# Performance work log

Hardware: AMD Instinct MI355X
Metric: run time of the kernel (lower is better)

Reference implementation:

```python
import jax, jax.numpy as jnp
import numpy as np

H = 512        # edge_feature_size (input_size == hidden_size)
B = 8          # batch
N = 8192       # n_nodes


def setup_inputs() -> dict:
    key = jax.random.key(0)
    k1, k2, k3, k4 = jax.random.split(key, 4)
    # Glorot-ish init scale like torch GRU (uniform +-1/sqrt(H))
    s = 1.0 / np.sqrt(H)
    e_wv = jax.random.normal(k1, (B, H, N), dtype=jnp.float32)
    m_wv = jax.random.normal(k2, (B, H, N), dtype=jnp.float32)
    # torch GRU weight layout: [3H, H] stacked as (reset, update, new)
    W_ih = jax.random.uniform(k3, (3 * H, H), dtype=jnp.float32, minval=-s, maxval=s)
    W_hh = jax.random.uniform(k4, (3 * H, H), dtype=jnp.float32, minval=-s, maxval=s)
    return {"e_wv": e_wv, "m_wv": m_wv, "W_ih": W_ih, "W_hh": W_hh}


def reference(e_wv, m_wv, W_ih, W_hh):
    # Single-step GRU cell (no bias), applied to all nodes at once.
    # e_wv: hidden state h0 [B, H, N]; m_wv: input x [B, H, N].
    gi = jnp.einsum('gh,bhn->bgn', W_ih, m_wv)   # [B, 3H, N]
    gh = jnp.einsum('gh,bhn->bgn', W_hh, e_wv)   # [B, 3H, N]
    i_r, i_z, i_n = gi[:, :H], gi[:, H:2 * H], gi[:, 2 * H:]
    h_r, h_z, h_n = gh[:, :H], gh[:, H:2 * H], gh[:, 2 * H:]
    r = jax.nn.sigmoid(i_r + h_r)
    z = jax.nn.sigmoid(i_z + h_z)
    n = jnp.tanh(i_n + r * h_n)
    return (1.0 - z) * n + z * e_wv              # [B, H, N]
```

## Files before the change

kernel.cpp:

```cpp
#include <hip/hip_runtime.h>
#include <hip/hip_bf16.h>


#define HH 512
#define NBATCH 8
#define NN 8192
#define BN 128
#define BK 64
#define NSTEPS 16
#define THREADS 256
#define A_BYTES (192 * BK * 2)
#define B_BYTES (BN * 128)
#define BUF_BYTES (A_BYTES + B_BYTES)
#define LDS_TOTAL (2 * BUF_BYTES)

#define WIMG_BYTES (NBATCH * NSTEPS * 12288 * 2)
#define XIMG_BYTES ((size_t)NBATCH * NSTEPS * 64 * 16384)
#define WS_NEED (WIMG_BYTES + XIMG_BYTES)

typedef __attribute__((ext_vector_type(8))) short short8;
typedef __attribute__((ext_vector_type(4))) float f32x4;

__device__ __forceinline__ unsigned cvt_pk_bf16(float a, float b) {
  unsigned r;
  asm("v_cvt_pk_bf16_f32 %0, %1, %2" : "=v"(r) : "v"(a), "v"(b));
  return r;
}

__device__ __forceinline__ void gload_lds16(const void* g, void* l) {
  __builtin_amdgcn_global_load_lds(
      (__attribute__((address_space(1))) void*)(g),
      (__attribute__((address_space(3))) void*)(l), 16, 0, 0);
}

#define MFMA16(a_, b_, c_) __builtin_amdgcn_mfma_f32_16x16x32_bf16((a_), (b_), (c_), 0, 0, 0)

#define BARRIER_FENCED() do {                               \
    __builtin_amdgcn_sched_barrier(0);                      \
    __builtin_amdgcn_s_barrier();                           \
    __builtin_amdgcn_sched_barrier(0);                      \
  } while (0)

__global__ void prepack_w(const float* __restrict__ W_ih, const float* __restrict__ W_hh,
                          __hip_bfloat16* __restrict__ ws) {
  int t = blockIdx.x * 256 + threadIdx.x;
  int blk = t / 12288;
  int e = t % 12288;
  int ra = e >> 6;
  int kk = (e & 63) ^ ((ra & 7) << 3);
  int gate = ra >> 6;
  int h = (blk >> 4) * 64 + (ra & 63);
  int row = gate * HH + h;
  int kg = (blk & 15) * 64 + kk;
  float v = (kg < 512) ? W_ih[row * 512 + kg] : W_hh[row * 512 + (kg - 512)];
  ws[t] = __float2bfloat16(v);
}

__global__ void prepack_x(const float* __restrict__ e_wv, const float* __restrict__ m_wv,
                          char* __restrict__ ximg) {
  __shared__ __align__(16) char tile[16384];
  const int tid = threadIdx.x;
  const int idx = blockIdx.x;
  const int b  = idx >> 10;
  const int s  = (idx >> 6) & 15;
  const int nt = idx & 63;
  const float* src = (s < 8 ? m_wv : e_wv)
                   + (size_t)b * HH * NN + (size_t)(64 * (s & 7)) * NN + nt * 128;
#pragma unroll
  for (int it = 0; it < 8; ++it) {
    int g = it * 256 + tid;
    int k = g >> 5;
    int n4 = (g & 31) << 2;
    f32x4 v = *(const f32x4*)(src + (size_t)k * NN + n4);
#pragma unroll
    for (int j = 0; j < 4; ++j) {
      int n = n4 + j;
      int byteoff = n * 128 + ((2 * k) ^ (((n >> 1) & 7) << 4));
      *(__hip_bfloat16*)(tile + byteoff) = __float2bfloat16(v[j]);
    }
  }
  __syncthreads();
  char* dst = ximg + (size_t)idx * 16384;
#pragma unroll
  for (int it = 0; it < 4; ++it) {
    int p = it * 4096 + tid * 16;
    *(uint4*)(dst + p) = *(const uint4*)(tile + p);
  }
}

__global__ __launch_bounds__(THREADS, 2)
void gru_main_dma(const float* __restrict__ e_wv,
                  const __hip_bfloat16* __restrict__ wimg,
                  const char* __restrict__ ximg, float* __restrict__ out) {
  extern __shared__ char smem[];
  const int tid  = threadIdx.x;
  const int lane = tid & 63;
  const int wave = tid >> 6;
  const int wm = wave >> 1;
  const int wn = wave & 1;

  const int wg  = blockIdx.x;
  const int swz = (wg & 7) * 512 + (wg >> 3);
  const int ht  = swz & 7;
  const int nt  = (swz >> 3) & 63;
  const int b   = swz >> 9;

  const size_t batch_off = (size_t)b * HH * NN;
  const char* wA  = (const char*)wimg + (size_t)ht * NSTEPS * A_BYTES + tid * 16;
  const char* xib = ximg + ((size_t)(b * 16) * 64 + nt) * 16384 + tid * 16;

  f32x4 acc_r[2][4]  = {};
  f32x4 acc_z[2][4]  = {};
  f32x4 acc_in[2][4] = {};
  f32x4 acc_hn[2][4] = {};

  int aoff[2], boff[2];
#pragma unroll
  for (int kb2 = 0; kb2 < 2; ++kb2) {
    const int K = kb2 * 64 + ((lane >> 4) << 4);
    aoff[kb2] = (wm * 32 + (lane & 15)) * 128 + (K ^ ((lane & 7) << 4));
    boff[kb2] = A_BYTES + (wn * 64 + (lane & 15)) * 128
              + (K ^ (((lane >> 1) & 7) << 4));
  }

  auto stage = [&](int t, char* buf) {
    const char* gA = wA + (size_t)t * A_BYTES;
    char* lA = buf + tid * 16;
#pragma unroll
    for (int i = 0; i < 6; ++i)
      gload_lds16(gA + i * 4096, lA + i * 4096);
    const char* gB = xib + (size_t)t * (64 * 16384);
    char* lB = buf + A_BYTES + tid * 16;
#pragma unroll
    for (int i = 0; i < 4; ++i)
      gload_lds16(gB + i * 4096, lB + i * 4096);
  };
  auto compute_kb2 = [&](const char* cb, int kb2, bool firstHalf) {
    short8 bfr[4];
#pragma unroll
    for (int ni = 0; ni < 4; ++ni)
      bfr[ni] = *(const short8*)(cb + boff[kb2] + ni * 2048);
    {
      short8 a0 = *(const short8*)(cb + aoff[kb2]);
      short8 a1 = *(const short8*)(cb + aoff[kb2] + 2048);
#pragma unroll
      for (int ni = 0; ni < 4; ++ni) {
        acc_r[0][ni] = MFMA16(a0, bfr[ni], acc_r[0][ni]);
        acc_r[1][ni] = MFMA16(a1, bfr[ni], acc_r[1][ni]);
      }
    }
    {
      short8 a0 = *(const short8*)(cb + aoff[kb2] + 8192);
      short8 a1 = *(const short8*)(cb + aoff[kb2] + 8192 + 2048);
#pragma unroll
      for (int ni = 0; ni < 4; ++ni) {
        acc_z[0][ni] = MFMA16(a0, bfr[ni], acc_z[0][ni]);
        acc_z[1][ni] = MFMA16(a1, bfr[ni], acc_z[1][ni]);
      }
    }
    {
      short8 a0 = *(const short8*)(cb + aoff[kb2] + 16384);
      short8 a1 = *(const short8*)(cb + aoff[kb2] + 16384 + 2048);
      if (firstHalf) {
#pragma unroll
        for (int ni = 0; ni < 4; ++ni) {
          acc_in[0][ni] = MFMA16(a0, bfr[ni], acc_in[0][ni]);
          acc_in[1][ni] = MFMA16(a1, bfr[ni], acc_in[1][ni]);
        }
      } else {
#pragma unroll
        for (int ni = 0; ni < 4; ++ni) {
          acc_hn[0][ni] = MFMA16(a0, bfr[ni], acc_hn[0][ni]);
          acc_hn[1][ni] = MFMA16(a1, bfr[ni], acc_hn[1][ni]);
        }
      }
    }
  };

  stage(0, smem);
  stage(1, smem + BUF_BYTES);
  asm volatile("s_waitcnt vmcnt(10)" ::: "memory");
  BARRIER_FENCED();

#pragma unroll 1
  for (int t = 0; t < NSTEPS; ++t) {
    char* cb = smem + ((t & 1) ? BUF_BYTES : 0);
    const bool firstHalf = (t < 8);

    compute_kb2(cb, 0, firstHalf);
    compute_kb2(cb, 1, firstHalf);

    asm volatile("s_waitcnt lgkmcnt(0)" ::: "memory");
    BARRIER_FENCED();

    if (t + 2 < NSTEPS) stage(t + 2, cb);

    if (t + 1 < NSTEPS) {
      if (t + 2 < NSTEPS)
        asm volatile("s_waitcnt vmcnt(10)" ::: "memory");
      else
        asm volatile("s_waitcnt vmcnt(0)" ::: "memory");
      BARRIER_FENCED();
    }
  }

  const size_t obase = batch_off + (size_t)(ht * 64 + wm * 32) * NN + nt * BN + wn * 64;
  const float* ep = e_wv + obase;
  float* op = out + obase;
  const int rsub = (lane >> 4) << 2;
  const int csub = lane & 15;
#pragma unroll
  for (int mi = 0; mi < 2; ++mi)
#pragma unroll
    for (int ni = 0; ni < 4; ++ni) {
#pragma unroll
      for (int r = 0; r < 4; ++r) {
        size_t idx = (size_t)(mi * 16 + rsub + r) * NN + ni * 16 + csub;
        float pr  = acc_r[mi][ni][r];
        float pz  = acc_z[mi][ni][r];
        float vin = acc_in[mi][ni][r];
        float vhn = acc_hn[mi][ni][r];
        float rr  = 1.f / (1.f + __expf(-pr));
        float zz  = 1.f / (1.f + __expf(-pz));
        float ex  = __expf(2.f * (vin + rr * vhn));
        float nn2 = 1.f - 2.f / (ex + 1.f);
        float ev  = ep[idx];
        op[idx] = (1.f - zz) * nn2 + zz * ev;
      }
    }
}

__global__ __launch_bounds__(THREADS, 2)
void gru_main_fb(const float* __restrict__ e_wv, const float* __restrict__ m_wv,
                 const __hip_bfloat16* __restrict__ wimg, float* __restrict__ out) {
  extern __shared__ char smem[];
  const int tid  = threadIdx.x;
  const int lane = tid & 63;
  const int wave = tid >> 6;
  const int wm = wave >> 1;
  const int wn = wave & 1;
  const int wg  = blockIdx.x;
  const int swz = (wg & 7) * 512 + (wg >> 3);
  const int ht  = swz & 7;
  const int nt  = (swz >> 3) & 63;
  const int b   = swz >> 9;
  const size_t batch_off = (size_t)b * HH * NN;
  const float* xm = m_wv + batch_off + (size_t)(16 * wave) * NN + nt * BN + 2 * lane;
  const float* xe = e_wv + batch_off + (size_t)(16 * wave) * NN + nt * BN + 2 * lane;
  const char*  wA = (const char*)wimg + (size_t)ht * NSTEPS * A_BYTES + tid * 16;
  f32x4 acc_r[2][4]  = {};
  f32x4 acc_z[2][4]  = {};
  f32x4 acc_in[2][4] = {};
  f32x4 acc_hn[2][4] = {};
  float2 xR[16];
  int aoff[2], boff[2];
#pragma unroll
  for (int kb2 = 0; kb2 < 2; ++kb2) {
    const int K = kb2 * 64 + ((lane >> 4) << 4);
    aoff[kb2] = (wm * 32 + (lane & 15)) * 128 + (K ^ ((lane & 7) << 4));
    boff[kb2] = A_BYTES + (wn * 64 + (lane & 15)) * 128 + (K ^ (((lane >> 1) & 7) << 4));
  }
  auto issue_A = [&](int s, char* nb) {
    const char* gA = wA + (size_t)s * A_BYTES;
    char* lA = nb + tid * 16;
#pragma unroll
    for (int i = 0; i < 6; ++i) gload_lds16(gA + i * 4096, lA + i * 4096);
  };
  auto x_load = [&](const float* xs) {
#pragma unroll
    for (int i = 0; i < 16; ++i) xR[i] = *(const float2*)(xs + (size_t)i * NN);
  };
  auto write_X = [&](char* nb) {
    char* Bb = nb + A_BYTES + (2 * lane) * 128;
    const int sx = (lane & 7) << 4;
#pragma unroll
    for (int o = 0; o < 2; ++o) {
      uint4 w0, w1;
      w0.x = cvt_pk_bf16(xR[8 * o + 0].x, xR[8 * o + 1].x);
      w0.y = cvt_pk_bf16(xR[8 * o + 2].x, xR[8 * o + 3].x);
      w0.z = cvt_pk_bf16(xR[8 * o + 4].x, xR[8 * o + 5].x);
      w0.w = cvt_pk_bf16(xR[8 * o + 6].x, xR[8 * o + 7].x);
      w1.x = cvt_pk_bf16(xR[8 * o + 0].y, xR[8 * o + 1].y);
      w1.y = cvt_pk_bf16(xR[8 * o + 2].y, xR[8 * o + 3].y);
      w1.z = cvt_pk_bf16(xR[8 * o + 4].y, xR[8 * o + 5].y);
      w1.w = cvt_pk_bf16(xR[8 * o + 6].y, xR[8 * o + 7].y);
      const int kb = (32 * wave + 16 * o) ^ sx;
      *(uint4*)(Bb + kb)       = w0;
      *(uint4*)(Bb + 128 + kb) = w1;
    }
  };
  auto compute_kb2 = [&](const char* cb, int kb2, bool firstHalf) {
    short8 bfr[4];
#pragma unroll
    for (int ni = 0; ni < 4; ++ni) bfr[ni] = *(const short8*)(cb + boff[kb2] + ni * 2048);
    {
      short8 a0 = *(const short8*)(cb + aoff[kb2]);
      short8 a1 = *(const short8*)(cb + aoff[kb2] + 2048);
#pragma unroll
      for (int ni = 0; ni < 4; ++ni) {
        acc_r[0][ni] = MFMA16(a0, bfr[ni], acc_r[0][ni]);
        acc_r[1][ni] = MFMA16(a1, bfr[ni], acc_r[1][ni]);
      }
    }
    {
      short8 a0 = *(const short8*)(cb + aoff[kb2] + 8192);
      short8 a1 = *(const short8*)(cb + aoff[kb2] + 8192 + 2048);
#pragma unroll
      for (int ni = 0; ni < 4; ++ni) {
        acc_z[0][ni] = MFMA16(a0, bfr[ni], acc_z[0][ni]);
        acc_z[1][ni] = MFMA16(a1, bfr[ni], acc_z[1][ni]);
      }
    }
    {
      short8 a0 = *(const short8*)(cb + aoff[kb2] + 16384);
      short8 a1 = *(const short8*)(cb + aoff[kb2] + 16384 + 2048);
      if (firstHalf) {
#pragma unroll
        for (int ni = 0; ni < 4; ++ni) {
          acc_in[0][ni] = MFMA16(a0, bfr[ni], acc_in[0][ni]);
          acc_in[1][ni] = MFMA16(a1, bfr[ni], acc_in[1][ni]);
        }
      } else {
#pragma unroll
        for (int ni = 0; ni < 4; ++ni) {
          acc_hn[0][ni] = MFMA16(a0, bfr[ni], acc_hn[0][ni]);
          acc_hn[1][ni] = MFMA16(a1, bfr[ni], acc_hn[1][ni]);
        }
      }
    }
  };
  issue_A(0, smem);
  x_load(xm);
  write_X(smem);
  __syncthreads();
#pragma unroll 1
  for (int s = 0; s < NSTEPS; ++s) {
    char* cb = smem + ((s & 1) ? BUF_BYTES : 0);
    char* nb = smem + ((s & 1) ? 0 : BUF_BYTES);
    const bool pre = (s < NSTEPS - 1);
    const bool firstHalf = (s < 8);
    if (pre) {
      const int t = s + 1;
      x_load((t < 8 ? xm : xe) + (size_t)(t & 7) * (64 * NN));
      issue_A(t, nb);
    }
    compute_kb2(cb, 0, firstHalf);
    compute_kb2(cb, 1, firstHalf);
    if (pre) write_X(nb);
    __syncthreads();
  }
  const size_t obase = batch_off + (size_t)(ht * 64 + wm * 32) * NN + nt * BN + wn * 64;
  const float* ep = e_wv + obase;
  float* op = out + obase;
  const int rsub = (lane >> 4) << 2;
  const int csub = lane & 15;
#pragma unroll
  for (int mi = 0; mi < 2; ++mi)
#pragma unroll
    for (int ni = 0; ni < 4; ++ni) {
#pragma unroll
      for (int r = 0; r < 4; ++r) {
        size_t idx = (size_t)(mi * 16 + rsub + r) * NN + ni * 16 + csub;
        float pr  = acc_r[mi][ni][r];
        float pz  = acc_z[mi][ni][r];
        float vin = acc_in[mi][ni][r];
        float vhn = acc_hn[mi][ni][r];
        float rr  = 1.f / (1.f + __expf(-pr));
        float zz  = 1.f / (1.f + __expf(-pz));
        float ex  = __expf(2.f * (vin + rr * vhn));
        float nn2 = 1.f - 2.f / (ex + 1.f);
        float ev  = ep[idx];
        op[idx] = (1.f - zz) * nn2 + zz * ev;
      }
    }
}

extern "C" void kernel_launch(void* const* d_in, const int* in_sizes, int n_in,
                              void* d_out, int out_size, void* d_ws, size_t ws_size,
                              hipStream_t stream) {
  const float* e_wv = (const float*)d_in[0];
  const float* m_wv = (const float*)d_in[1];
  const float* W_ih = (const float*)d_in[2];
  const float* W_hh = (const float*)d_in[3];
  float* out = (float*)d_out;
  __hip_bfloat16* wimg = (__hip_bfloat16*)d_ws;
  char* ximg = (char*)d_ws + WIMG_BYTES;

  (void)hipFuncSetAttribute((const void*)gru_main_dma,
                            hipFuncAttributeMaxDynamicSharedMemorySize, LDS_TOTAL);
  (void)hipFuncSetAttribute((const void*)gru_main_fb,
                            hipFuncAttributeMaxDynamicSharedMemorySize, LDS_TOTAL);

  prepack_w<<<(NBATCH * NSTEPS * 12288) / 256, 256, 0, stream>>>(W_ih, W_hh, wimg);

  if (ws_size >= WS_NEED) {
    prepack_x<<<NBATCH * NSTEPS * 64, 256, 0, stream>>>(e_wv, m_wv, ximg);
    gru_main_dma<<<NBATCH * 8 * 64, THREADS, LDS_TOTAL, stream>>>(e_wv, wimg, ximg, out);
  } else {
    gru_main_fb<<<NBATCH * 8 * 64, THREADS, LDS_TOTAL, stream>>>(e_wv, m_wv, wimg, out);
  }
}
```

Baseline: 309.0 us.

## Load weight fragments directly from global memory and triple-buffer activation tiles in LDS

Weights are prepacked into a per-lane MFMA fragment layout, so each wave reads its A operands straight from global memory (L2-resident) instead of staging them through LDS. LDS now holds only the activation tiles, which allows a three-buffer ring with a single barrier per step instead of two. This cuts LDS traffic and footprint, which may raise occupancy and remove one sync per step. The cost is latency-exposed global loads on the MFMA critical path and heavier L2 traffic, since weights are re-read per workgroup.

```diff
diff --git a/kernel.cpp b/kernel.cpp
--- a/kernel.cpp
+++ b/kernel.cpp
@@ -6,13 +6,13 @@
 #define NBATCH 8
 #define NN 8192
 #define BN 128
-#define BK 64
 #define NSTEPS 16
 #define THREADS 256
-#define A_BYTES (192 * BK * 2)
-#define B_BYTES (BN * 128)
-#define BUF_BYTES (A_BYTES + B_BYTES)
-#define LDS_TOTAL (2 * BUF_BYTES)
+#define BBUF 16384
+#define LDS_DMA (3 * BBUF)
+#define A_BYTES (192 * 64 * 2)
+#define FB_BUF (A_BYTES + BBUF)
+#define LDS_FB (2 * FB_BUF)
 
 #define WIMG_BYTES (NBATCH * NSTEPS * 12288 * 2)
 #define XIMG_BYTES ((size_t)NBATCH * NSTEPS * 64 * 16384)
@@ -34,6 +34,7 @@
 }
 
 #define MFMA16(a_, b_, c_) __builtin_amdgcn_mfma_f32_16x16x32_bf16((a_), (b_), (c_), 0, 0, 0)
+#define LD8(p) (*(const short8*)(p))
 
 #define BARRIER_FENCED() do {                               \
     __builtin_amdgcn_sched_barrier(0);                      \
@@ -41,8 +42,29 @@
     __builtin_amdgcn_sched_barrier(0);                      \
   } while (0)
 
-__global__ void prepack_w(const float* __restrict__ W_ih, const float* __restrict__ W_hh,
-                          __hip_bfloat16* __restrict__ ws) {
+__global__ void prepack_w_frag(const float* __restrict__ W_ih,
+                               const float* __restrict__ W_hh,
+                               __hip_bfloat16* __restrict__ ws) {
+  int t = blockIdx.x * 256 + threadIdx.x;
+  int lane = t & 63; int u = t >> 6;
+  int mi = u & 1;   u >>= 1;
+  int gate = u % 3; u /= 3;
+  int kb2 = u & 1;  u >>= 1;
+  int wm = u & 1;   u >>= 1;
+  int s = u & 15;   u >>= 4;
+  int ht = u;
+  int grow = gate * HH + ht * 64 + wm * 32 + mi * 16 + (lane & 15);
+  int kg = s * 64 + kb2 * 32 + ((lane >> 4) << 3);
+  const float* src = (kg < 512) ? (W_ih + (size_t)grow * 512 + kg)
+                                : (W_hh + (size_t)grow * 512 + (kg - 512));
+  unsigned w[4];
+#pragma unroll
+  for (int j = 0; j < 4; ++j) w[j] = cvt_pk_bf16(src[2 * j], src[2 * j + 1]);
+  *(uint4*)((char*)ws + (size_t)t * 16) = make_uint4(w[0], w[1], w[2], w[3]);
+}
+
+__global__ void prepack_w_lds(const float* __restrict__ W_ih, const float* __restrict__ W_hh,
+                              __hip_bfloat16* __restrict__ ws) {
   int t = blockIdx.x * 256 + threadIdx.x;
   int blk = t / 12288;
   int e = t % 12288;
@@ -106,7 +128,7 @@
   const int b   = swz >> 9;
 
   const size_t batch_off = (size_t)b * HH * NN;
-  const char* wA  = (const char*)wimg + (size_t)ht * NSTEPS * A_BYTES + tid * 16;
+  const char* wA  = (const char*)wimg + ((size_t)(ht * 16) * 2 + wm) * 12288 + lane * 16;
   const char* xib = ximg + ((size_t)(b * 16) * 64 + nt) * 16384 + tid * 16;
 
   f32x4 acc_r[2][4]  = {};
@@ -114,94 +136,88 @@
   f32x4 acc_in[2][4] = {};
   f32x4 acc_hn[2][4] = {};
 
-  int aoff[2], boff[2];
+  int boff[2];
 #pragma unroll
   for (int kb2 = 0; kb2 < 2; ++kb2) {
     const int K = kb2 * 64 + ((lane >> 4) << 4);
-    aoff[kb2] = (wm * 32 + (lane & 15)) * 128 + (K ^ ((lane & 7) << 4));
-    boff[kb2] = A_BYTES + (wn * 64 + (lane & 15)) * 128
-              + (K ^ (((lane >> 1) & 7) << 4));
+    boff[kb2] = (wn * 64 + (lane & 15)) * 128 + (K ^ (((lane >> 1) & 7) << 4));
   }
 
   auto stage = [&](int t, char* buf) {
-    const char* gA = wA + (size_t)t * A_BYTES;
-    char* lA = buf + tid * 16;
-#pragma unroll
-    for (int i = 0; i < 6; ++i)
-      gload_lds16(gA + i * 4096, lA + i * 4096);
     const char* gB = xib + (size_t)t * (64 * 16384);
-    char* lB = buf + A_BYTES + tid * 16;
+    char* lB = buf + tid * 16;
 #pragma unroll
     for (int i = 0; i < 4; ++i)
       gload_lds16(gB + i * 4096, lB + i * 4096);
   };
-  auto compute_kb2 = [&](const char* cb, int kb2, bool firstHalf) {
-    short8 bfr[4];
-#pragma unroll
-    for (int ni = 0; ni < 4; ++ni)
-      bfr[ni] = *(const short8*)(cb + boff[kb2] + ni * 2048);
-    {
-      short8 a0 = *(const short8*)(cb + aoff[kb2]);
-      short8 a1 = *(const short8*)(cb + aoff[kb2] + 2048);
-#pragma unroll
-      for (int ni = 0; ni < 4; ++ni) {
-        acc_r[0][ni] = MFMA16(a0, bfr[ni], acc_r[0][ni]);
-        acc_r[1][ni] = MFMA16(a1, bfr[ni], acc_r[1][ni]);
-      }
-    }
-    {
-      short8 a0 = *(const short8*)(cb + aoff[kb2] + 8192);
-      short8 a1 = *(const short8*)(cb + aoff[kb2] + 8192 + 2048);
-#pragma unroll
-      for (int ni = 0; ni < 4; ++ni) {
-        acc_z[0][ni] = MFMA16(a0, bfr[ni], acc_z[0][ni]);
-        acc_z[1][ni] = MFMA16(a1, bfr[ni], acc_z[1][ni]);
-      }
-    }
-    {
-      short8 a0 = *(const short8*)(cb + aoff[kb2] + 16384);
-      short8 a1 = *(const short8*)(cb + aoff[kb2] + 16384 + 2048);
-      if (firstHalf) {
+  auto compute_step = [&](const char* cb, int s, bool firstHalf) {
+    const char* aS = wA + (size_t)s * 24576;
+#pragma unroll
+    for (int kb2 = 0; kb2 < 2; ++kb2) {
+      const char* aK = aS + kb2 * 6144;
+      short8 bfr[4];
+#pragma unroll
+      for (int ni = 0; ni < 4; ++ni)
+        bfr[ni] = LD8(cb + boff[kb2] + ni * 2048);
+      {
+        short8 a0 = LD8(aK);
+        short8 a1 = LD8(aK + 1024);
 #pragma unroll
         for (int ni = 0; ni < 4; ++ni) {
-          acc_in[0][ni] = MFMA16(a0, bfr[ni], acc_in[0][ni]);
-          acc_in[1][ni] = MFMA16(a1, bfr[ni], acc_in[1][ni]);
+          acc_r[0][ni] = MFMA16(a0, bfr[ni], acc_r[0][ni]);
+          acc_r[1][ni] = MFMA16(a1, bfr[ni], acc_r[1][ni]);
         }
-      } else {
+      }
+      {
+        short8 a0 = LD8(aK + 2048);
+        short8 a1 = LD8(aK + 3072);
 #pragma unroll
         for (int ni = 0; ni < 4; ++ni) {
-          acc_hn[0][ni] = MFMA16(a0, bfr[ni], acc_hn[0][ni]);
-          acc_hn[1][ni] = MFMA16(a1, bfr[ni], acc_hn[1][ni]);
+          acc_z[0][ni] = MFMA16(a0, bfr[ni], acc_z[0][ni]);
+          acc_z[1][ni] = MFMA16(a1, bfr[ni], acc_z[1][ni]);
         }
       }
+      {
+        short8 a0 = LD8(aK + 4096);
+        short8 a1 = LD8(aK + 5120);
+        if (firstHalf) {
+#pragma unroll
+          for (int ni = 0; ni < 4; ++ni) {
+            acc_in[0][ni] = MFMA16(a0, bfr[ni], acc_in[0][ni]);
+            acc_in[1][ni] = MFMA16(a1, bfr[ni], acc_in[1][ni]);
+          }
+        } else {
+#pragma unroll
+          for (int ni = 0; ni < 4; ++ni) {
+            acc_hn[0][ni] = MFMA16(a0, bfr[ni], acc_hn[0][ni]);
+            acc_hn[1][ni] = MFMA16(a1, bfr[ni], acc_hn[1][ni]);
+          }
+        }
+      }
     }
   };
 
   stage(0, smem);
-  stage(1, smem + BUF_BYTES);
-  asm volatile("s_waitcnt vmcnt(10)" ::: "memory");
+  stage(1, smem + BBUF);
+  asm volatile("s_waitcnt vmcnt(4)" ::: "memory");
   BARRIER_FENCED();
 
 #pragma unroll 1
   for (int t = 0; t < NSTEPS; ++t) {
-    char* cb = smem + ((t & 1) ? BUF_BYTES : 0);
+    char* cb = smem + (t % 3) * BBUF;
     const bool firstHalf = (t < 8);
 
-    compute_kb2(cb, 0, firstHalf);
-    compute_kb2(cb, 1, firstHalf);
-
-    asm volatile("s_waitcnt lgkmcnt(0)" ::: "memory");
-    BARRIER_FENCED();
-
-    if (t + 2 < NSTEPS) stage(t + 2, cb);
-
-    if (t + 1 < NSTEPS) {
-      if (t + 2 < NSTEPS)
-        asm volatile("s_waitcnt vmcnt(10)" ::: "memory");
-      else
-        asm volatile("s_waitcnt vmcnt(0)" ::: "memory");
-      BARRIER_FENCED();
-    }
+    compute_step(cb, t, firstHalf);
+
+    __builtin_amdgcn_sched_barrier(0);
+    if (t + 2 < NSTEPS) {
+      stage(t + 2, smem + ((t + 2) % 3) * BBUF);
+      __builtin_amdgcn_sched_barrier(0);
+      asm volatile("s_waitcnt vmcnt(4) lgkmcnt(0)" ::: "memory");
+    } else {
+      asm volatile("s_waitcnt vmcnt(0) lgkmcnt(0)" ::: "memory");
+    }
+    if (t < NSTEPS - 1) BARRIER_FENCED();
   }
 
   const size_t obase = batch_off + (size_t)(ht * 64 + wm * 32) * NN + nt * BN + wn * 64;
@@ -335,8 +351,8 @@
   __syncthreads();
 #pragma unroll 1
   for (int s = 0; s < NSTEPS; ++s) {
-    char* cb = smem + ((s & 1) ? BUF_BYTES : 0);
-    char* nb = smem + ((s & 1) ? 0 : BUF_BYTES);
+    char* cb = smem + ((s & 1) ? FB_BUF : 0);
+    char* nb = smem + ((s & 1) ? 0 : FB_BUF);
     const bool pre = (s < NSTEPS - 1);
     const bool firstHalf = (s < 8);
     if (pre) {
@@ -387,16 +403,16 @@
   char* ximg = (char*)d_ws + WIMG_BYTES;
 
   (void)hipFuncSetAttribute((const void*)gru_main_dma,
-                            hipFuncAttributeMaxDynamicSharedMemorySize, LDS_TOTAL);
+                            hipFuncAttributeMaxDynamicSharedMemorySize, LDS_DMA);
   (void)hipFuncSetAttribute((const void*)gru_main_fb,
-                            hipFuncAttributeMaxDynamicSharedMemorySize, LDS_TOTAL);
-
-  prepack_w<<<(NBATCH * NSTEPS * 12288) / 256, 256, 0, stream>>>(W_ih, W_hh, wimg);
+                            hipFuncAttributeMaxDynamicSharedMemorySize, LDS_FB);
 
   if (ws_size >= WS_NEED) {
+    prepack_w_frag<<<196608 / 256, 256, 0, stream>>>(W_ih, W_hh, wimg);
     prepack_x<<<NBATCH * NSTEPS * 64, 256, 0, stream>>>(e_wv, m_wv, ximg);
-    gru_main_dma<<<NBATCH * 8 * 64, THREADS, LDS_TOTAL, stream>>>(e_wv, wimg, ximg, out);
+    gru_main_dma<<<NBATCH * 8 * 64, THREADS, LDS_DMA, stream>>>(e_wv, wimg, ximg, out);
   } else {
-    gru_main_fb<<<NBATCH * 8 * 64, THREADS, LDS_TOTAL, stream>>>(e_wv, m_wv, wimg, out);
-  }
-}
+    prepack_w_lds<<<(NBATCH * NSTEPS * 12288) / 256, 256, 0, stream>>>(W_ih, W_hh, wimg);
+    gru_main_fb<<<NBATCH * 8 * 64, THREADS, LDS_FB, stream>>>(e_wv, m_wv, wimg, out);
+  }
+}
```

After: 414.4 us. 1.34x slower.
